# Optimization experiments

Hardware: AMD Instinct MI355X
Metric: run time of the kernel (lower is better)

## Reference

```python
import jax, jax.numpy as jnp
import numpy as np

DIM = 48
D_STATE = 16
D_CONV = 4
EXPAND = 2
D_INNER = DIM * EXPAND          # 96
DT_RANK = (DIM + 15) // 16      # 3
EPS = 1e-5


def _interp2x_align_corners(x, axis):
    """Linear 2x upsample along one axis with align_corners=True."""
    n = x.shape[axis]
    out = 2 * n
    pos = jnp.arange(out, dtype=jnp.float32) * (n - 1) / (out - 1)
    lo = jnp.floor(pos).astype(jnp.int32)
    hi = jnp.minimum(lo + 1, n - 1)
    w = (pos - lo.astype(jnp.float32)).astype(x.dtype)
    shape = [1] * x.ndim
    shape[axis] = out
    w = w.reshape(shape)
    return jnp.take(x, lo, axis=axis) * (1 - w) + jnp.take(x, hi, axis=axis) * w


def _upsample_trilinear2x(x):
    for axis in (2, 3, 4):
        x = _interp2x_align_corners(x, axis)
    return x


def _conv3d(x, w, b, pad):
    y = jax.lax.conv_general_dilated(
        x, w, window_strides=(1, 1, 1), padding=[(pad, pad)] * 3,
        dimension_numbers=('NCDHW', 'OIDHW', 'NCDHW'))
    return y + b[None, :, None, None, None]


def _instance_norm(x):
    m = x.mean(axis=(2, 3, 4), keepdims=True)
    v = x.var(axis=(2, 3, 4), keepdims=True)  # biased var, as PyTorch InstanceNorm3d
    return (x - m) / jnp.sqrt(v + EPS)


def _mamba(u, in_proj_w, conv1d_w, conv1d_b, x_proj_w, dt_proj_w, dt_proj_b,
           A_log, D_param, out_proj_w):
    # u: (B, L, d_model)
    Bsz, L, _ = u.shape
    xz = jnp.einsum('bld,ed->ble', u, in_proj_w)        # (B, L, 2*Di)
    xi, z = jnp.split(xz, 2, axis=-1)                   # each (B, L, Di)
    # depthwise causal conv1d (pad left d_conv-1, crop to L == mamba's slice)
    xpad = jnp.pad(xi.transpose(0, 2, 1), ((0, 0), (0, 0), (D_CONV - 1, 0)))
    xc = jax.lax.conv_general_dilated(
        xpad, conv1d_w, window_strides=(1,), padding=[(0, 0)],
        dimension_numbers=('NCH', 'OIH', 'NCH'), feature_group_count=D_INNER)
    xs = jax.nn.silu((xc + conv1d_b[None, :, None]).transpose(0, 2, 1))  # (B, L, Di)

    dbc = jnp.einsum('bld,ed->ble', xs, x_proj_w)       # (B, L, dt_rank+2*N)
    dt, Bm, Cm = jnp.split(dbc, [DT_RANK, DT_RANK + D_STATE], axis=-1)
    delta = jax.nn.softplus(jnp.einsum('blr,dr->bld', dt, dt_proj_w) + dt_proj_b)

    A = -jnp.exp(A_log)                                  # (Di, N)
    dA = jnp.exp(jnp.einsum('bld,dn->bldn', delta, A))   # (B, L, Di, N)
    dBx = jnp.einsum('bld,bln->bldn', delta * xs, Bm)    # (B, L, Di, N)

    def step(h, inp):
        dA_t, dBx_t, C_t = inp                           # (B,Di,N),(B,Di,N),(B,N)
        h = dA_t * h + dBx_t
        y = jnp.einsum('bdn,bn->bd', h, C_t)
        return h, y

    h0 = jnp.zeros((Bsz, D_INNER, D_STATE), xs.dtype)
    _, ys = jax.lax.scan(step, h0,
                         (dA.transpose(1, 0, 2, 3), dBx.transpose(1, 0, 2, 3),
                          Cm.transpose(1, 0, 2)))
    y = ys.transpose(1, 0, 2) + D_param[None, None, :] * xs
    y = y * jax.nn.silu(z)
    return jnp.einsum('bld,ed->ble', y, out_proj_w)      # (B, L, d_model)


def setup_inputs() -> dict:
    key = jax.random.key(0)
    ks = jax.random.split(key, 16)
    s = 0.05
    f32 = jnp.float32
    inp = {
        'x': jax.random.normal(ks[0], (2, DIM, 12, 12, 12), f32),
        'Hx': jax.random.normal(ks[1], (2, DIM * 2, 24, 24, 24), f32),
        'W1': jax.random.normal(ks[2], (DIM, DIM * 3, 1, 1, 1), f32) * s,
        'b1': jax.random.normal(ks[3], (DIM,), f32) * s,
        'W2': jax.random.normal(ks[4], (DIM, DIM, 3, 3, 3), f32) * s,
        'b2': jax.random.normal(ks[5], (DIM,), f32) * s,
        'W3': jax.random.normal(ks[6], (DIM, DIM, 1, 1, 1), f32) * s,
        'b3': jax.random.normal(ks[7], (DIM,), f32) * s,
        'in_proj_w': jax.random.normal(ks[8], (2 * D_INNER, DIM), f32) * s,
        'conv1d_w': jax.random.normal(ks[9], (D_INNER, 1, D_CONV), f32) * s,
        'conv1d_b': jax.random.normal(ks[10], (D_INNER,), f32) * s,
        'x_proj_w': jax.random.normal(ks[11], (DT_RANK + 2 * D_STATE, D_INNER), f32) * s,
        'dt_proj_w': jax.random.normal(ks[12], (D_INNER, DT_RANK), f32) * s,
        'dt_proj_b': jax.random.normal(ks[13], (D_INNER,), f32) * 0.1,
        'A_log': jnp.log(jnp.tile(jnp.arange(1, D_STATE + 1, dtype=f32)[None, :],
                                  (D_INNER, 1))),
        'D_param': jnp.ones((D_INNER,), f32),
        'out_proj_w': jax.random.normal(ks[14], (DIM, D_INNER), f32) * s,
    }
    return inp


def reference(x, Hx, W1, b1, W2, b2, W3, b3, in_proj_w, conv1d_w, conv1d_b,
              x_proj_w, dt_proj_w, dt_proj_b, A_log, D_param, out_proj_w):
    up = _upsample_trilinear2x(x)                         # (B, dim, 2H, 2W, 2T)
    h = jnp.concatenate([up, Hx], axis=1)                 # (B, 3*dim, ...)
    h = _conv3d(h, W1, b1, 0)
    h = _conv3d(h, W2, b2, 1)
    h = _conv3d(h, W3, b3, 0)
    Lx = jax.nn.selu(_instance_norm(h))
    B, C, H, W, T = Lx.shape
    u = Lx.reshape(B, C, H * W * T).transpose(0, 2, 1)    # (B, L, C)
    ym = _mamba(u, in_proj_w, conv1d_w, conv1d_b, x_proj_w, dt_proj_w,
                dt_proj_b, A_log, D_param, out_proj_w)
    out = ym.transpose(0, 2, 1).reshape(B, C, H, W, T) + Lx
    return out
```

## Files before the change

### kernel.cpp

```cpp
#include <hip/hip_runtime.h>
#include <math.h>

#define NB 2
#define NCH 48
#define P 13824
#define DI 96
#define NSTATE 16
#define L 13824
#define CHUNK 64
#define NCK 216
#define TL 32

__device__ __forceinline__ float siluf(float x) { return x / (1.f + __expf(-x)); }
__device__ __forceinline__ float softplusf(float x) {
    return x > 0.f ? x + log1pf(expf(-x)) : log1pf(expf(x));
}

__global__ __launch_bounds__(256) void k_wtrans(const float* __restrict__ W2,
    const float* __restrict__ W1, const float* __restrict__ W3,
    const float* __restrict__ Wop, float* __restrict__ Wt, float* __restrict__ W1t,
    float* __restrict__ W3t, float* __restrict__ Wopt)
{
    int i = blockIdx.x * 256 + threadIdx.x;
    if (i < 62208) {
        int o = i / (48 * 27); int r = i % (48 * 27); int c = r / 27; int tap = r % 27;
        int og = o / 12, oi = o % 12;
        Wt[(((og * 27 + tap) * 48 + c) * 12) + oi] = W2[i];
    } else if (i < 62208 + 6912) {
        int j = i - 62208; int o = j / 144, c = j % 144;
        W1t[c * 48 + o] = W1[j];
    } else if (i < 62208 + 6912 + 2304) {
        int j = i - 62208 - 6912; int o = j / 48, c = j % 48;
        W3t[c * 48 + o] = W3[j];
    } else if (i < 62208 + 6912 + 2304 + 4608) {
        int j = i - 62208 - 6912 - 2304; int o = j / 96, q = j % 96;
        Wopt[q * 48 + o] = Wop[j];
    }
}

__global__ __launch_bounds__(128) void k_conv1(const float* __restrict__ x,
    const float* __restrict__ Hx, const float* __restrict__ W1t,
    const float* __restrict__ b1, float* __restrict__ h1)
{
    int t = blockIdx.x * 128 + threadIdx.x;
    int oh = blockIdx.y * 12;
    int b = t / P, p = t % P;
    int zi = p / 576, yi = (p / 24) % 24, xi_ = p % 24;
    float fpos; int z0, z1, y0, y1, x0, x1; float wz, wy, wx;
    fpos = (float)(zi * 11) / 23.0f; z0 = (int)floorf(fpos); wz = fpos - z0; z1 = min(z0 + 1, 11);
    fpos = (float)(yi * 11) / 23.0f; y0 = (int)floorf(fpos); wy = fpos - y0; y1 = min(y0 + 1, 11);
    fpos = (float)(xi_ * 11) / 23.0f; x0 = (int)floorf(fpos); wx = fpos - x0; x1 = min(x0 + 1, 11);
    int o000 = (z0*12+y0)*12+x0, o001 = (z0*12+y0)*12+x1;
    int o010 = (z0*12+y1)*12+x0, o011 = (z0*12+y1)*12+x1;
    int o100 = (z1*12+y0)*12+x0, o101 = (z1*12+y0)*12+x1;
    int o110 = (z1*12+y1)*12+x0, o111 = (z1*12+y1)*12+x1;
    float uz = 1.f - wz, uy = 1.f - wy, ux = 1.f - wx;
    float w000 = uz*uy*ux, w001 = uz*uy*wx, w010 = uz*wy*ux, w011 = uz*wy*wx;
    float w100 = wz*uy*ux, w101 = wz*uy*wx, w110 = wz*wy*ux, w111 = wz*wy*wx;

    float acc[12];
#pragma unroll
    for (int o = 0; o < 12; ++o) acc[o] = b1[oh + o];
    const float* xb = x + (size_t)b * 48 * 1728;
    for (int c0 = 0; c0 < 48; c0 += 4) {
        float a[4][8];
#pragma unroll
        for (int j = 0; j < 4; ++j) {
            const float* xc = xb + (c0 + j) * 1728;
            a[j][0] = xc[o000]; a[j][1] = xc[o001]; a[j][2] = xc[o010]; a[j][3] = xc[o011];
            a[j][4] = xc[o100]; a[j][5] = xc[o101]; a[j][6] = xc[o110]; a[j][7] = xc[o111];
        }
#pragma unroll
        for (int j = 0; j < 4; ++j) {
            float v = a[j][0]*w000 + a[j][1]*w001 + a[j][2]*w010 + a[j][3]*w011
                    + a[j][4]*w100 + a[j][5]*w101 + a[j][6]*w110 + a[j][7]*w111;
            const float* wr = W1t + (c0 + j) * 48 + oh;
#pragma unroll
            for (int o = 0; o < 12; ++o) acc[o] = fmaf(wr[o], v, acc[o]);
        }
    }
    const float* hb = Hx + (size_t)b * 96 * P + p;
    for (int c0 = 0; c0 < 96; c0 += 8) {
        float v[8];
#pragma unroll
        for (int j = 0; j < 8; ++j) v[j] = hb[(size_t)(c0 + j) * P];
#pragma unroll
        for (int j = 0; j < 8; ++j) {
            const float* wr = W1t + (48 + c0 + j) * 48 + oh;
#pragma unroll
            for (int o = 0; o < 12; ++o) acc[o] = fmaf(wr[o], v[j], acc[o]);
        }
    }
    float* out = h1 + (size_t)b * 48 * P + p;
#pragma unroll
    for (int o = 0; o < 12; ++o) out[(size_t)(oh+o) * P] = acc[o];
}

__global__ __launch_bounds__(512) void k_conv23(const float* __restrict__ h1,
    const float* __restrict__ Wt, const float* __restrict__ b2,
    const float* __restrict__ W3t, const float* __restrict__ b3,
    float* __restrict__ h3)
{
    __shared__ float tile[216 * 52];
    int blk = blockIdx.x;
    int b = blk / 216; int r = blk % 216;
    int tz = r / 36, ty = (r / 6) % 6, tx = r % 6;
    int z0 = tz*4 - 1, y0 = ty*4 - 1, x0 = tx*4 - 1;
    for (int i = threadIdx.x; i < 216 * 12; i += 512) {
        int q = i % 216; int c4 = (i / 216) * 4;
        int lz = q / 36, ly = (q / 6) % 6, lx = q % 6;
        int gz = z0 + lz, gy = y0 + ly, gx = x0 + lx;
        float4 v = {0.f, 0.f, 0.f, 0.f};
        if ((unsigned)gz < 24u && (unsigned)gy < 24u && (unsigned)gx < 24u) {
            size_t gp = (size_t)(gz*24 + gy)*24 + gx;
            const float* hp = h1 + ((size_t)(b*48 + c4)) * P + gp;
            v.x = hp[0];
            v.y = hp[P];
            v.z = hp[2*P];
            v.w = hp[3*P];
        }
        *(float4*)(&tile[q*52 + c4]) = v;
    }
    __syncthreads();
    int lp = threadIdx.x & 63;
    int w  = __builtin_amdgcn_readfirstlane((int)(threadIdx.x >> 6));
    int og = w & 3, cc = w >> 2;
    int lz = lp >> 4, ly = (lp >> 2) & 3, lx = lp & 3;
    float acc[12];
#pragma unroll
    for (int i = 0; i < 12; ++i) acc[i] = cc ? 0.f : b2[og*12 + i];
#pragma unroll
    for (int dz = 0; dz < 3; ++dz)
#pragma unroll
    for (int dy = 0; dy < 3; ++dy)
#pragma unroll
    for (int dx = 0; dx < 3; ++dx) {
        int pos = (lz+dz)*36 + (ly+dy)*6 + (lx+dx);
        const float* tp = tile + pos*52 + cc*24;
        int tap = (dz*3 + dy)*3 + dx;
        const float* wt = Wt + (((size_t)og*27 + tap)*48 + cc*24)*12;
#pragma unroll
        for (int cq = 0; cq < 6; ++cq) {
            float4 v4 = *(const float4*)(tp + cq*4);
            const float* wq = wt + cq*48;
#pragma unroll
            for (int i = 0; i < 12; ++i) {
                acc[i] = fmaf(wq[i],      v4.x, acc[i]);
                acc[i] = fmaf(wq[12 + i], v4.y, acc[i]);
                acc[i] = fmaf(wq[24 + i], v4.z, acc[i]);
                acc[i] = fmaf(wq[36 + i], v4.w, acc[i]);
            }
        }
    }
    __syncthreads();
    if (cc == 1) {
        float* ex = tile + og * 768;
#pragma unroll
        for (int i = 0; i < 12; ++i) ex[i*64 + lp] = acc[i];
    }
    __syncthreads();
    if (cc == 0) {
        const float* ex = tile + og * 768;
        float* ht = tile + 3072;
#pragma unroll
        for (int i = 0; i < 12; ++i)
            ht[(og*12 + i)*64 + lp] = acc[i] + ex[i*64 + lp];
    }
    __syncthreads();
    const float* ht = tile + 3072;
    int oc0 = w * 6;
    float acc3[6];
#pragma unroll
    for (int j = 0; j < 6; ++j) acc3[j] = b3[oc0 + j];
    for (int c = 0; c < 48; ++c) {
        float v = ht[c*64 + lp];
        const float* wr = W3t + c*48 + oc0;
#pragma unroll
        for (int j = 0; j < 6; ++j) acc3[j] = fmaf(wr[j], v, acc3[j]);
    }
    int gz = tz*4 + lz, gy = ty*4 + ly, gx = tx*4 + lx;
    size_t pp = (size_t)(gz*24 + gy)*24 + gx;
#pragma unroll
    for (int j = 0; j < 6; ++j)
        h3[((size_t)(b*48) + oc0 + j) * P + pp] = acc3[j];
}

__global__ __launch_bounds__(1024) void k_instnorm(float* __restrict__ h3)
{
    int bc = blockIdx.x;
    float4* src = (float4*)(h3 + (size_t)bc * P);
    float s = 0.f, s2 = 0.f;
    for (int i = threadIdx.x; i < 3456; i += 1024) {
        float4 v = src[i];
        s  += v.x + v.y + v.z + v.w;
        s2 += v.x*v.x + v.y*v.y + v.z*v.z + v.w*v.w;
    }
    __shared__ float rs[16], rs2[16], mv[2];
    for (int off = 32; off; off >>= 1) { s += __shfl_down(s, off); s2 += __shfl_down(s2, off); }
    int wid = threadIdx.x >> 6;
    if ((threadIdx.x & 63) == 0) { rs[wid] = s; rs2[wid] = s2; }
    __syncthreads();
    if (threadIdx.x == 0) {
        s = 0.f; s2 = 0.f;
#pragma unroll
        for (int k = 0; k < 16; ++k) { s += rs[k]; s2 += rs2[k]; }
        float m = s / (float)P;
        float var = s2 / (float)P - m * m;
        mv[0] = m; mv[1] = rsqrtf(var + 1e-5f);
    }
    __syncthreads();
    float m = mv[0], istd = mv[1];
    const float kS = 1.0507009873554805f, kA = 1.6732632423543772f;
    for (int i = threadIdx.x; i < 3456; i += 1024) {
        float4 v = src[i];
        float a0 = (v.x - m) * istd, a1 = (v.y - m) * istd;
        float a2 = (v.z - m) * istd, a3 = (v.w - m) * istd;
        v.x = a0 > 0.f ? kS * a0 : kS * kA * expm1f(a0);
        v.y = a1 > 0.f ? kS * a1 : kS * kA * expm1f(a1);
        v.z = a2 > 0.f ? kS * a2 : kS * kA * expm1f(a2);
        v.w = a3 > 0.f ? kS * a3 : kS * kA * expm1f(a3);
        src[i] = v;
    }
}

__global__ __launch_bounds__(192) void k_inproj(const float* __restrict__ Lx,
    const float* __restrict__ Wip, float* __restrict__ xi, float* __restrict__ z)
{
    int b = blockIdx.x / 576; int l0 = (blockIdx.x % 576) * 24;
    int e = threadIdx.x;
    float w[48];
#pragma unroll
    for (int c = 0; c < 48; ++c) w[c] = Wip[e*48 + c];
    float acc[24];
#pragma unroll
    for (int ll = 0; ll < 24; ++ll) acc[ll] = 0.f;
    const float* ub = Lx + (size_t)b * 48 * P + l0;
#pragma unroll 2
    for (int c = 0; c < 48; ++c) {
        const float* ur = ub + (size_t)c * P;
#pragma unroll
        for (int ll = 0; ll < 24; ++ll) acc[ll] = fmaf(w[c], ur[ll], acc[ll]);
    }
    float* dst = (e < 96) ? (xi + ((size_t)b * L + l0) * 96 + e)
                          : (z  + ((size_t)b * L + l0) * 96 + (e - 96));
#pragma unroll
    for (int ll = 0; ll < 24; ++ll) dst[(size_t)ll * 96] = acc[ll];
}

__global__ __launch_bounds__(256) void k_fxproj(const float* __restrict__ xi,
    const float* __restrict__ cw, const float* __restrict__ cb,
    const float* __restrict__ Wxp, const float* __restrict__ Wdt,
    const float* __restrict__ bdt, float* __restrict__ xs,
    float* __restrict__ delta, float* __restrict__ Bm, float* __restrict__ Cm)
{
    __shared__ float xs_t[TL][100];
    __shared__ float wx_t[35][100];
    __shared__ float wd_t[96][4];
    __shared__ float dt_t[TL][4];
    int blk = blockIdx.x;
    int b = blk / 432; int l0 = (blk % 432) * TL;
    int tid = threadIdx.x;

    for (int i = tid; i < 35 * 96; i += 256) wx_t[i / 96][i % 96] = Wxp[i];
    for (int i = tid; i < 96 * 3; i += 256) wd_t[i / 3][i % 3] = Wdt[i];
    for (int i = tid; i < 96; i += 256) wd_t[i][3] = bdt[i];

    int row = tid >> 3;
    int q8  = tid & 7;
    int d0  = q8 * 12;
    int l = l0 + row;
    size_t t_glob = (size_t)b * L + l;
    const float* xib = xi + (size_t)b * L * 96;
    float* xsg = xs + t_glob * 96 + d0;
    int ls0 = l - 3;
#pragma unroll
    for (int jq = 0; jq < 3; ++jq) {
        int d = d0 + jq * 4;
        float4 t0 = *(const float4*)(cw + 4 * (d + 0));
        float4 t1 = *(const float4*)(cw + 4 * (d + 1));
        float4 t2 = *(const float4*)(cw + 4 * (d + 2));
        float4 t3 = *(const float4*)(cw + 4 * (d + 3));
        float4 acc = *(const float4*)(cb + d);
        float4 q0 = {0.f,0.f,0.f,0.f}, q1 = q0, q2 = q0;
        if (ls0 + 0 >= 0) q0 = *(const float4*)(xib + (size_t)(ls0 + 0) * 96 + d);
        if (ls0 + 1 >= 0) q1 = *(const float4*)(xib + (size_t)(ls0 + 1) * 96 + d);
        if (ls0 + 2 >= 0) q2 = *(const float4*)(xib + (size_t)(ls0 + 2) * 96 + d);
        float4 q3 = *(const float4*)(xib + (size_t)(ls0 + 3) * 96 + d);
        acc.x += t0.x*q0.x + t0.y*q1.x + t0.z*q2.x + t0.w*q3.x;
        acc.y += t1.x*q0.y + t1.y*q1.y + t1.z*q2.y + t1.w*q3.y;
        acc.z += t2.x*q0.z + t2.y*q1.z + t2.z*q2.z + t2.w*q3.z;
        acc.w += t3.x*q0.w + t3.y*q1.w + t3.z*q2.w + t3.w*q3.w;
        acc.x = siluf(acc.x); acc.y = siluf(acc.y);
        acc.z = siluf(acc.z); acc.w = siluf(acc.w);
        *(float4*)(&xs_t[row][d0 + jq * 4]) = acc;
        *(float4*)(xsg + jq * 4) = acc;
    }
    __syncthreads();

    float acc5[5];
#pragma unroll
    for (int k = 0; k < 5; ++k) acc5[k] = 0.f;
    const float* xrow = &xs_t[row][0];
#pragma unroll 4
    for (int j = 0; j < 24; ++j) {
        float4 xv = *(const float4*)(xrow + 4 * j);
#pragma unroll
        for (int k = 0; k < 5; ++k) {
            int e = q8 + 8 * k;
            if (e < 35) {
                float4 wv = *(const float4*)(&wx_t[e][4 * j]);
                acc5[k] = fmaf(wv.x, xv.x, fmaf(wv.y, xv.y,
                          fmaf(wv.z, xv.z, fmaf(wv.w, xv.w, acc5[k]))));
            }
        }
    }
#pragma unroll
    for (int k = 0; k < 5; ++k) {
        int e = q8 + 8 * k;
        if (e < 35) {
            if (e < 3)       dt_t[row][e] = acc5[k];
            else if (e < 19) Bm[t_glob * 16 + (e - 3)]  = acc5[k];
            else             Cm[t_glob * 16 + (e - 19)] = acc5[k];
        }
    }
    __syncthreads();

    float dt0 = dt_t[row][0], dt1 = dt_t[row][1], dt2 = dt_t[row][2];
    float* dl = delta + t_glob * 96 + d0;
#pragma unroll
    for (int jq = 0; jq < 3; ++jq) {
        float4 o;
        {
            float4 wv = *(const float4*)(&wd_t[d0 + jq*4 + 0][0]);
            o.x = softplusf(fmaf(wv.x, dt0, fmaf(wv.y, dt1, fmaf(wv.z, dt2, wv.w))));
        }
        {
            float4 wv = *(const float4*)(&wd_t[d0 + jq*4 + 1][0]);
            o.y = softplusf(fmaf(wv.x, dt0, fmaf(wv.y, dt1, fmaf(wv.z, dt2, wv.w))));
        }
        {
            float4 wv = *(const float4*)(&wd_t[d0 + jq*4 + 2][0]);
            o.z = softplusf(fmaf(wv.x, dt0, fmaf(wv.y, dt1, fmaf(wv.z, dt2, wv.w))));
        }
        {
            float4 wv = *(const float4*)(&wd_t[d0 + jq*4 + 3][0]);
            o.w = softplusf(fmaf(wv.x, dt0, fmaf(wv.y, dt1, fmaf(wv.z, dt2, wv.w))));
        }
        *(float4*)(dl + jq * 4) = o;
    }
}

__global__ __launch_bounds__(256) void k_scan1(const float* __restrict__ delta,
    const float* __restrict__ xs, const float* __restrict__ Bm,
    const float* __restrict__ Alog, float* __restrict__ Aprod, float* __restrict__ hend)
{
    int wid = (blockIdx.x * 256 + threadIdx.x) >> 6;
    int lane = threadIdx.x & 63;
    int dg = wid % 24; int ch = (wid / 24) % NCK; int b = wid / (24 * NCK);
    int dl = lane >> 4, n = lane & 15;
    int d = dg * 4 + dl;
    float A = -__expf(Alog[d*16 + n]);
    float h = 0.f, ap = 1.f;
    int t0 = ch * CHUNK;
    const float* dp = delta + ((size_t)b * L + t0) * 96 + d;
    const float* xp = xs    + ((size_t)b * L + t0) * 96 + d;
    const float* bp = Bm    + ((size_t)b * L + t0) * 16 + n;

    float dA0, dA1, dA2, dA3, xA0, xA1, xA2, xA3, bA0, bA1, bA2, bA3;
    float dB0, dB1, dB2, dB3, xB0, xB1, xB2, xB3, bB0, bB1, bB2, bB3;
#define LD1(s, T) do { \
    d##s##0 = dp[(size_t)(T)*96];     x##s##0 = xp[(size_t)(T)*96];     b##s##0 = bp[(size_t)(T)*16]; \
    d##s##1 = dp[(size_t)((T)+1)*96]; x##s##1 = xp[(size_t)((T)+1)*96]; b##s##1 = bp[(size_t)((T)+1)*16]; \
    d##s##2 = dp[(size_t)((T)+2)*96]; x##s##2 = xp[(size_t)((T)+2)*96]; b##s##2 = bp[(size_t)((T)+2)*16]; \
    d##s##3 = dp[(size_t)((T)+3)*96]; x##s##3 = xp[(size_t)((T)+3)*96]; b##s##3 = bp[(size_t)((T)+3)*16]; \
  } while (0)
#define CMP1(s) do { \
    float e0 = __expf(d##s##0 * A); float e1 = __expf(d##s##1 * A); \
    float e2 = __expf(d##s##2 * A); float e3 = __expf(d##s##3 * A); \
    h = fmaf(e0, h, d##s##0 * x##s##0 * b##s##0); \
    h = fmaf(e1, h, d##s##1 * x##s##1 * b##s##1); \
    h = fmaf(e2, h, d##s##2 * x##s##2 * b##s##2); \
    h = fmaf(e3, h, d##s##3 * x##s##3 * b##s##3); \
    ap *= e0 * e1 * e2 * e3; \
  } while (0)

    LD1(A, 0);
#pragma unroll 1
    for (int t = 0; t < CHUNK; t += 8) {
        LD1(B, t + 4);
        CMP1(A);
        if (t + 8 < CHUNK) LD1(A, t + 8);
        CMP1(B);
    }
#undef LD1
#undef CMP1
    size_t idx = (((size_t)b * NCK + ch) * 96 + d) * 16 + n;
    Aprod[idx] = ap;
    hend[idx]  = h;
}

__global__ __launch_bounds__(256) void k_scan2(const float* __restrict__ Aprod,
    const float* __restrict__ hend, float* __restrict__ hin)
{
    int t = blockIdx.x * 256 + threadIdx.x;
    int b = t / 1536; int dn = t % 1536;
    const float* ap = Aprod + (size_t)b * NCK * 1536 + dn;
    const float* he = hend  + (size_t)b * NCK * 1536 + dn;
    float* hi       = hin   + (size_t)b * NCK * 1536 + dn;
    float carry = 0.f;
    float aA0, aA1, aA2, aA3, hA0, hA1, hA2, hA3;
    float aB0, aB1, aB2, aB3, hB0, hB1, hB2, hB3;
#define LD2(s, J) do { \
    a##s##0 = ap[(size_t)(J)*1536];     h##s##0 = he[(size_t)(J)*1536]; \
    a##s##1 = ap[(size_t)((J)+1)*1536]; h##s##1 = he[(size_t)((J)+1)*1536]; \
    a##s##2 = ap[(size_t)((J)+2)*1536]; h##s##2 = he[(size_t)((J)+2)*1536]; \
    a##s##3 = ap[(size_t)((J)+3)*1536]; h##s##3 = he[(size_t)((J)+3)*1536]; \
  } while (0)
#define CMP2(s, J) do { \
    hi[(size_t)(J)*1536]     = carry; carry = fmaf(a##s##0, carry, h##s##0); \
    hi[(size_t)((J)+1)*1536] = carry; carry = fmaf(a##s##1, carry, h##s##1); \
    hi[(size_t)((J)+2)*1536] = carry; carry = fmaf(a##s##2, carry, h##s##2); \
    hi[(size_t)((J)+3)*1536] = carry; carry = fmaf(a##s##3, carry, h##s##3); \
  } while (0)
    LD2(A, 0);
#pragma unroll 1
    for (int j = 0; j < NCK; j += 8) {
        LD2(B, j + 4);
        CMP2(A, j);
        if (j + 8 < NCK) LD2(A, j + 8);
        CMP2(B, j + 4);
    }
#undef LD2
#undef CMP2
}

__global__ __launch_bounds__(256) void k_scan3(const float* __restrict__ delta,
    float* __restrict__ xs, const float* __restrict__ Bm, const float* __restrict__ Cm,
    const float* __restrict__ z, const float* __restrict__ Alog,
    const float* __restrict__ Dp, const float* __restrict__ hin)
{
    int wid = (blockIdx.x * 256 + threadIdx.x) >> 6;
    int lane = threadIdx.x & 63;
    int dg = wid % 24; int ch = (wid / 24) % NCK; int b = wid / (24 * NCK);
    int dl = lane >> 4, n = lane & 15;
    int d = dg * 4 + dl;
    float A = -__expf(Alog[d*16 + n]);
    float Dv = Dp[d];
    size_t cidx = (((size_t)b * NCK + ch) * 96 + d) * 16 + n;
    float h = hin[cidx];
    int t0 = ch * CHUNK;
    const float* dp = delta + ((size_t)b * L + t0) * 96 + d;
    float* xp       = xs    + ((size_t)b * L + t0) * 96 + d;
    const float* bp = Bm    + ((size_t)b * L + t0) * 16 + n;
    const float* cp = Cm    + ((size_t)b * L + t0) * 16 + n;
    const float* zp = z     + ((size_t)b * L + t0) * 96 + d;

    float dA0, dA1, dA2, dA3, xA0, xA1, xA2, xA3, bA0, bA1, bA2, bA3, cA0, cA1, cA2, cA3, zA0, zA1, zA2, zA3;
    float dB0, dB1, dB2, dB3, xB0, xB1, xB2, xB3, bB0, bB1, bB2, bB3, cB0, cB1, cB2, cB3, zB0, zB1, zB2, zB3;
#define LD3(s, T) do { \
    d##s##0 = dp[(size_t)(T)*96];     x##s##0 = xp[(size_t)(T)*96];     b##s##0 = bp[(size_t)(T)*16]; \
    c##s##0 = cp[(size_t)(T)*16];     z##s##0 = zp[(size_t)(T)*96]; \
    d##s##1 = dp[(size_t)((T)+1)*96]; x##s##1 = xp[(size_t)((T)+1)*96]; b##s##1 = bp[(size_t)((T)+1)*16]; \
    c##s##1 = cp[(size_t)((T)+1)*16]; z##s##1 = zp[(size_t)((T)+1)*96]; \
    d##s##2 = dp[(size_t)((T)+2)*96]; x##s##2 = xp[(size_t)((T)+2)*96]; b##s##2 = bp[(size_t)((T)+2)*16]; \
    c##s##2 = cp[(size_t)((T)+2)*16]; z##s##2 = zp[(size_t)((T)+2)*96]; \
    d##s##3 = dp[(size_t)((T)+3)*96]; x##s##3 = xp[(size_t)((T)+3)*96]; b##s##3 = bp[(size_t)((T)+3)*16]; \
    c##s##3 = cp[(size_t)((T)+3)*16]; z##s##3 = zp[(size_t)((T)+3)*96]; \
  } while (0)
#define STEP3(DEL, XV, BV, CV, ZV, T) do { \
    float dAv = __expf((DEL) * A); \
    h = fmaf(dAv, h, (DEL) * (XV) * (BV)); \
    float yc = h * (CV); \
    yc += __shfl_xor(yc, 8); \
    yc += __shfl_xor(yc, 4); \
    yc += __shfl_xor(yc, 2); \
    yc += __shfl_xor(yc, 1); \
    if (n == 0) xp[(size_t)(T)*96] = fmaf(Dv, (XV), yc) * siluf(ZV); \
  } while (0)
#define CMP3(s, T) do { \
    STEP3(d##s##0, x##s##0, b##s##0, c##s##0, z##s##0, (T)); \
    STEP3(d##s##1, x##s##1, b##s##1, c##s##1, z##s##1, (T)+1); \
    STEP3(d##s##2, x##s##2, b##s##2, c##s##2, z##s##2, (T)+2); \
    STEP3(d##s##3, x##s##3, b##s##3, c##s##3, z##s##3, (T)+3); \
  } while (0)

    LD3(A, 0);
#pragma unroll 1
    for (int t = 0; t < CHUNK; t += 8) {
        LD3(B, t + 4);
        CMP3(A, t);
        if (t + 8 < CHUNK) LD3(A, t + 8);
        CMP3(B, t + 4);
    }
#undef LD3
#undef STEP3
#undef CMP3
}

__global__ __launch_bounds__(128) void k_outproj(const float* __restrict__ y,
    const float* __restrict__ Wopt, const float* __restrict__ Lx, float* __restrict__ out)
{
    int t = blockIdx.x * 128 + threadIdx.x;
    int oh = blockIdx.y * 12;
    int b = t / P, p = t % P;
    const float* yr = y + (size_t)t * 96;
    float acc[12];
#pragma unroll
    for (int o = 0; o < 12; ++o) acc[o] = 0.f;
#pragma unroll
    for (int i = 0; i < 24; ++i) {
        float4 v4 = ((const float4*)yr)[i];
        const float* w0 = Wopt + (i*4) * 48 + oh;
        const float* w1 = Wopt + (i*4 + 1) * 48 + oh;
        const float* w2 = Wopt + (i*4 + 2) * 48 + oh;
        const float* w3 = Wopt + (i*4 + 3) * 48 + oh;
#pragma unroll
        for (int o = 0; o < 12; ++o) {
            acc[o] = fmaf(w0[o], v4.x, acc[o]);
            acc[o] = fmaf(w1[o], v4.y, acc[o]);
            acc[o] = fmaf(w2[o], v4.z, acc[o]);
            acc[o] = fmaf(w3[o], v4.w, acc[o]);
        }
    }
    const float* lx = Lx + (size_t)b * 48 * P + p;
    float* op = out + (size_t)b * 48 * P + p;
#pragma unroll
    for (int o = 0; o < 12; ++o) op[(size_t)(oh+o) * P] = acc[o] + lx[(size_t)(oh+o) * P];
}

extern "C" void kernel_launch(void* const* d_in, const int* in_sizes, int n_in,
                              void* d_out, int out_size, void* d_ws, size_t ws_size,
                              hipStream_t stream) {
    const float* x        = (const float*)d_in[0];
    const float* Hx       = (const float*)d_in[1];
    const float* W1       = (const float*)d_in[2];
    const float* b1       = (const float*)d_in[3];
    const float* W2       = (const float*)d_in[4];
    const float* b2       = (const float*)d_in[5];
    const float* W3       = (const float*)d_in[6];
    const float* b3       = (const float*)d_in[7];
    const float* in_proj  = (const float*)d_in[8];
    const float* conv1d_w = (const float*)d_in[9];
    const float* conv1d_b = (const float*)d_in[10];
    const float* x_proj   = (const float*)d_in[11];
    const float* dt_proj  = (const float*)d_in[12];
    const float* dt_bias  = (const float*)d_in[13];
    const float* A_log    = (const float*)d_in[14];
    const float* D_param  = (const float*)d_in[15];
    const float* out_proj = (const float*)d_in[16];
    float* out = (float*)d_out;

    float* ws = (float*)d_ws;
    const size_t SZ_BCP = (size_t)NB * 48 * P;
    const size_t SZ_BLD = (size_t)NB * L * 96;
    const size_t SZ_BLN = (size_t)NB * L * 16;
    const size_t SZ_CK  = (size_t)NB * NCK * 1536;
    float* bufA  = ws;
    float* bufB  = bufA + SZ_BCP;
    float* bufC  = bufB + SZ_BCP;
    float* xib   = bufC + SZ_BCP;
    float* zb    = xib  + SZ_BLD;
    float* xsb   = zb   + SZ_BLD;
    float* Bmb   = xsb  + SZ_BLD;
    float* Cmb   = Bmb  + SZ_BLN;
    float* stats = Cmb  + SZ_BLN;
    float* Wtb   = stats + 192;
    float* W1tb  = Wtb + 62208;
    float* W3tb  = W1tb + 6912;
    float* Woptb = W3tb + 2304;
    float* deltab = bufA;
    float* Apr   = xib;
    float* hendb = xib + SZ_CK;
    float* hinb  = xib + 2 * SZ_CK;

    k_wtrans<<<297, 256, 0, stream>>>(W2, W1, W3, out_proj, Wtb, W1tb, W3tb, Woptb);
    k_conv1<<<dim3(216, 4), 128, 0, stream>>>(x, Hx, W1tb, b1, bufA);
    k_conv23<<<NB * 216, 512, 0, stream>>>(bufA, Wtb, b2, W3tb, b3, bufC);
    k_instnorm<<<NB * 48, 1024, 0, stream>>>(bufC);
    k_inproj<<<NB * 576, 192, 0, stream>>>(bufC, in_proj, xib, zb);
    k_fxproj<<<NB * 432, 256, 0, stream>>>(xib, conv1d_w, conv1d_b, x_proj, dt_proj,
                                           dt_bias, xsb, deltab, Bmb, Cmb);
    k_scan1<<<(NB * NCK * 24) / 4, 256, 0, stream>>>(deltab, xsb, Bmb, A_log, Apr, hendb);
    k_scan2<<<12, 256, 0, stream>>>(Apr, hendb, hinb);
    k_scan3<<<(NB * NCK * 24) / 4, 256, 0, stream>>>(deltab, xsb, Bmb, Cmb, zb, A_log,
                                                     D_param, hinb);
    k_outproj<<<dim3(216, 4), 128, 0, stream>>>(xsb, Woptb, bufC, out);
}
```

Measured before the change: 261.8 us.

## Split conv2+conv3 block across two output halves with partial sums merged in instnorm

```diff
diff --git a/kernel.cpp b/kernel.cpp
--- a/kernel.cpp
+++ b/kernel.cpp
@@ -96,17 +96,18 @@
     for (int o = 0; o < 12; ++o) out[(size_t)(oh+o) * P] = acc[o];
 }
 
-__global__ __launch_bounds__(512) void k_conv23(const float* __restrict__ h1,
+__global__ __launch_bounds__(256) void k_conv23(const float* __restrict__ h1,
     const float* __restrict__ Wt, const float* __restrict__ b2,
     const float* __restrict__ W3t, const float* __restrict__ b3,
-    float* __restrict__ h3)
+    float* __restrict__ h3a, float* __restrict__ h3b)
 {
     __shared__ float tile[216 * 52];
     int blk = blockIdx.x;
+    int oh = blockIdx.y;
     int b = blk / 216; int r = blk % 216;
     int tz = r / 36, ty = (r / 6) % 6, tx = r % 6;
     int z0 = tz*4 - 1, y0 = ty*4 - 1, x0 = tx*4 - 1;
-    for (int i = threadIdx.x; i < 216 * 12; i += 512) {
+    for (int i = threadIdx.x; i < 216 * 12; i += 256) {
         int q = i % 216; int c4 = (i / 216) * 4;
         int lz = q / 36, ly = (q / 6) % 6, lx = q % 6;
         int gz = z0 + lz, gy = y0 + ly, gx = x0 + lx;
@@ -124,7 +125,7 @@
     __syncthreads();
     int lp = threadIdx.x & 63;
     int w  = __builtin_amdgcn_readfirstlane((int)(threadIdx.x >> 6));
-    int og = w & 3, cc = w >> 2;
+    int og = oh * 2 + (w & 1), cc = w >> 1;
     int lz = lp >> 4, ly = (lp >> 2) & 3, lx = lp & 3;
     float acc[12];
 #pragma unroll
@@ -154,46 +155,50 @@
     }
     __syncthreads();
     if (cc == 1) {
-        float* ex = tile + og * 768;
+        float* ex = tile + (w & 1) * 768;
 #pragma unroll
         for (int i = 0; i < 12; ++i) ex[i*64 + lp] = acc[i];
     }
     __syncthreads();
     if (cc == 0) {
-        const float* ex = tile + og * 768;
-        float* ht = tile + 3072;
+        const float* ex = tile + (w & 1) * 768;
+        float* ht = tile + 1536;
 #pragma unroll
         for (int i = 0; i < 12; ++i)
-            ht[(og*12 + i)*64 + lp] = acc[i] + ex[i*64 + lp];
-    }
-    __syncthreads();
-    const float* ht = tile + 3072;
-    int oc0 = w * 6;
-    float acc3[6];
-#pragma unroll
-    for (int j = 0; j < 6; ++j) acc3[j] = b3[oc0 + j];
-    for (int c = 0; c < 48; ++c) {
+            ht[((w & 1)*12 + i)*64 + lp] = acc[i] + ex[i*64 + lp];
+    }
+    __syncthreads();
+    const float* ht = tile + 1536;
+    int oc0 = w * 12;
+    float acc3[12];
+#pragma unroll
+    for (int j = 0; j < 12; ++j) acc3[j] = (oh == 0) ? b3[oc0 + j] : 0.f;
+    for (int c = 0; c < 24; ++c) {
         float v = ht[c*64 + lp];
-        const float* wr = W3t + c*48 + oc0;
-#pragma unroll
-        for (int j = 0; j < 6; ++j) acc3[j] = fmaf(wr[j], v, acc3[j]);
-    }
+        const float* wr = W3t + (oh*24 + c)*48 + oc0;
+#pragma unroll
+        for (int j = 0; j < 12; ++j) acc3[j] = fmaf(wr[j], v, acc3[j]);
+    }
+    float* dst = oh ? h3b : h3a;
     int gz = tz*4 + lz, gy = ty*4 + ly, gx = tx*4 + lx;
     size_t pp = (size_t)(gz*24 + gy)*24 + gx;
 #pragma unroll
-    for (int j = 0; j < 6; ++j)
-        h3[((size_t)(b*48) + oc0 + j) * P + pp] = acc3[j];
-}
-
-__global__ __launch_bounds__(1024) void k_instnorm(float* __restrict__ h3)
+    for (int j = 0; j < 12; ++j)
+        dst[((size_t)(b*48) + oc0 + j) * P + pp] = acc3[j];
+}
+
+__global__ __launch_bounds__(1024) void k_instnorm(float* __restrict__ h3a,
+                                                   const float* __restrict__ h3b)
 {
     int bc = blockIdx.x;
-    float4* src = (float4*)(h3 + (size_t)bc * P);
+    float4* src  = (float4*)(h3a + (size_t)bc * P);
+    const float4* src2 = (const float4*)(h3b + (size_t)bc * P);
     float s = 0.f, s2 = 0.f;
     for (int i = threadIdx.x; i < 3456; i += 1024) {
-        float4 v = src[i];
-        s  += v.x + v.y + v.z + v.w;
-        s2 += v.x*v.x + v.y*v.y + v.z*v.z + v.w*v.w;
+        float4 v = src[i]; float4 u = src2[i];
+        float a0 = v.x + u.x, a1 = v.y + u.y, a2 = v.z + u.z, a3 = v.w + u.w;
+        s  += a0 + a1 + a2 + a3;
+        s2 += a0*a0 + a1*a1 + a2*a2 + a3*a3;
     }
     __shared__ float rs[16], rs2[16], mv[2];
     for (int off = 32; off; off >>= 1) { s += __shfl_down(s, off); s2 += __shfl_down(s2, off); }
@@ -212,9 +217,9 @@
     float m = mv[0], istd = mv[1];
     const float kS = 1.0507009873554805f, kA = 1.6732632423543772f;
     for (int i = threadIdx.x; i < 3456; i += 1024) {
-        float4 v = src[i];
-        float a0 = (v.x - m) * istd, a1 = (v.y - m) * istd;
-        float a2 = (v.z - m) * istd, a3 = (v.w - m) * istd;
+        float4 v = src[i]; float4 u = src2[i];
+        float a0 = (v.x + u.x - m) * istd, a1 = (v.y + u.y - m) * istd;
+        float a2 = (v.z + u.z - m) * istd, a3 = (v.w + u.w - m) * istd;
         v.x = a0 > 0.f ? kS * a0 : kS * kA * expm1f(a0);
         v.y = a1 > 0.f ? kS * a1 : kS * kA * expm1f(a1);
         v.z = a2 > 0.f ? kS * a2 : kS * kA * expm1f(a2);
@@ -575,8 +580,8 @@
 
     k_wtrans<<<297, 256, 0, stream>>>(W2, W1, W3, out_proj, Wtb, W1tb, W3tb, Woptb);
     k_conv1<<<dim3(216, 4), 128, 0, stream>>>(x, Hx, W1tb, b1, bufA);
-    k_conv23<<<NB * 216, 512, 0, stream>>>(bufA, Wtb, b2, W3tb, b3, bufC);
-    k_instnorm<<<NB * 48, 1024, 0, stream>>>(bufC);
+    k_conv23<<<dim3(NB * 216, 2), 256, 0, stream>>>(bufA, Wtb, b2, W3tb, b3, bufC, bufB);
+    k_instnorm<<<NB * 48, 1024, 0, stream>>>(bufC, bufB);
     k_inproj<<<NB * 576, 192, 0, stream>>>(bufC, in_proj, xib, zb);
     k_fxproj<<<NB * 432, 256, 0, stream>>>(xib, conv1d_w, conv1d_b, x_proj, dt_proj,
                                            dt_bias, xsb, deltab, Bmb, Cmb);
```

Result: slower. 303.1 us (+15.8%).
